# Kernel optimization log

Hardware: AMD Instinct MI355X
Metric: run time of the kernel (lower is better)

## Reference

```python
import jax, jax.numpy as jnp
import numpy as np

N_EMB = 384
BLOCK_SIZE = 256


def setup_inputs() -> dict:
    key = jax.random.key(0)
    ks = jax.random.split(key, 6)
    B, T, H, D = 256, 256, 6, 64
    x = jax.random.normal(ks[0], (B, T, N_EMB), dtype=jnp.float32)
    wk = jax.random.normal(ks[1], (H, N_EMB, D), dtype=jnp.float32) * (N_EMB ** -0.5)
    wq = jax.random.normal(ks[2], (H, N_EMB, D), dtype=jnp.float32) * (N_EMB ** -0.5)
    wv = jax.random.normal(ks[3], (H, N_EMB, D), dtype=jnp.float32) * (N_EMB ** -0.5)
    wproj = jax.random.normal(ks[4], (N_EMB, N_EMB), dtype=jnp.float32) * (N_EMB ** -0.5)
    bproj = jnp.zeros((N_EMB,), dtype=jnp.float32)
    return {"x": x, "wk": wk, "wq": wq, "wv": wv, "wproj": wproj, "bproj": bproj}


def reference(x, wk, wq, wv, wproj, bproj):
    B, T, C = x.shape  # C == N_EMB
    # per-head projections (no bias), heads stacked on leading axis
    k = jnp.einsum('btc,hcd->bhtd', x, wk)
    q = jnp.einsum('btc,hcd->bhtd', x, wq)
    v = jnp.einsum('btc,hcd->bhtd', x, wv)
    # faithful to source: wei = k @ q^T scaled by sqrt(C) (embed dim, not head dim)
    wei = jnp.einsum('bhtd,bhsd->bhts', k, q) / (C ** 0.5)
    causal = jnp.tril(jnp.ones((T, T), dtype=bool))
    wei = jnp.where(causal, wei, -jnp.inf)
    wei = jax.nn.softmax(wei, axis=-1)
    # dropout is identity in eval mode
    out = jnp.einsum('bhts,bhsd->bhtd', wei, v)  # [B,H,T,D]
    out = out.transpose(0, 2, 1, 3).reshape(B, T, C)  # concat heads
    out = out @ wproj + bproj
    return out
```

## Files before the change

### kernel.cpp

```cpp
#include <hip/hip_runtime.h>

typedef unsigned short u16;
typedef __bf16 bf16x8 __attribute__((ext_vector_type(8)));
typedef float f32x4 __attribute__((ext_vector_type(4)));

#define B_SZ 256
#define T_SZ 256
#define C_EMB 384
#define NHEAD 6
#define DHEAD 64
#define N3 1152
#define BHTD 25165824
#define SCALE 0.05103103630798287f
#define MASKV -3.0e4f

__device__ __forceinline__ u16 f2bf(float f) {
  __bf16 b = (__bf16)f;
  return __builtin_bit_cast(u16, b);
}

__device__ __forceinline__ void gload_lds16(const void* g, void* l) {
  __builtin_amdgcn_global_load_lds((const __attribute__((address_space(1))) void*)g,
                                   (__attribute__((address_space(3))) void*)l, 16, 0, 0);
}

__global__ __launch_bounds__(256) void prep_all(
    const float* __restrict__ x, const float* __restrict__ wk,
    const float* __restrict__ wq, const float* __restrict__ wv,
    const float* __restrict__ wproj,
    u16* __restrict__ xb, u16* __restrict__ wqkvt, u16* __restrict__ wprojt) {
  int bidx = blockIdx.x;
  if (bidx < 12288) {
    int i = bidx * 256 + threadIdx.x;
    float4 f0 = ((const float4*)x)[i * 2];
    float4 f1 = ((const float4*)x)[i * 2 + 1];
    uint4 p;
    p.x = (unsigned)f2bf(f0.x) | ((unsigned)f2bf(f0.y) << 16);
    p.y = (unsigned)f2bf(f0.z) | ((unsigned)f2bf(f0.w) << 16);
    p.z = (unsigned)f2bf(f1.x) | ((unsigned)f2bf(f1.y) << 16);
    p.w = (unsigned)f2bf(f1.z) | ((unsigned)f2bf(f1.w) << 16);
    ((uint4*)xb)[i] = p;
  } else {
    int i = (bidx - 12288) * 256 + threadIdx.x;
    if (i < N3 * C_EMB) {
      int n = i / C_EMB, c = i - n * C_EMB;
      int tensor = n >= 768 ? 2 : (n >= 384 ? 1 : 0);
      int r = n - tensor * 384;
      int h = r >> 6, d = r & 63;
      const float* w = tensor == 0 ? wk : (tensor == 1 ? wq : wv);
      float val = w[(h * C_EMB + c) * DHEAD + d];
      if (tensor == 0) val *= SCALE;
      wqkvt[i] = f2bf(val);
    } else {
      int ii = i - N3 * C_EMB;
      if (ii < C_EMB * C_EMB) {
        int n = ii / C_EMB, c = ii - n * C_EMB;
        wprojt[ii] = f2bf(wproj[c * C_EMB + n]);
      }
    }
  }
}

__global__ __launch_bounds__(256, 4) void qkv_gemm(const u16* __restrict__ xb,
                                                   const u16* __restrict__ wt,
                                                   u16* __restrict__ kqv) {
  __shared__ __align__(16) u16 lA[128 * 64];
  __shared__ __align__(16) u16 lB[128 * 64];
  const int tid = threadIdx.x;
  const int lane = tid & 63, w = tid >> 6;
  int bid = blockIdx.x;
  int nb = (bid & 7) * 576 + (bid >> 3);
  int mt = nb / 9, nt = nb - mt * 9;
  const int n0 = nt * 128, m0 = mt * 128;
  const int wr = w >> 1, wc = w & 1;
  f32x4 acc[4][4] = {};
  for (int kt = 0; kt < 6; ++kt) {
    const int k0 = kt * 64;
#pragma unroll
    for (int it = 0; it < 4; ++it) {
      int ub = it * 256 + w * 64;
      int u = ub + lane;
      int row = u >> 3, cu = u & 7;
      int koff = k0 + ((cu ^ (row & 7)) << 3);
      gload_lds16(xb + (size_t)(m0 + row) * C_EMB + koff, lA + ub * 8);
      gload_lds16(wt + (size_t)(n0 + row) * C_EMB + koff, lB + ub * 8);
    }
    asm volatile("s_waitcnt vmcnt(0)" ::: "memory");
    asm volatile("s_barrier" ::: "memory");
    bf16x8 af[4][2], bfr[4][2];
#pragma unroll
    for (int mi = 0; mi < 4; ++mi) {
      int row = wr * 64 + mi * 16 + (lane & 15);
#pragma unroll
      for (int kk = 0; kk < 2; ++kk) {
        int cu = kk * 4 + (lane >> 4);
        af[mi][kk] = *(const bf16x8*)((const char*)lA + row * 128 + ((cu ^ (row & 7)) << 4));
      }
    }
#pragma unroll
    for (int ni = 0; ni < 4; ++ni) {
      int row = wc * 64 + ni * 16 + (lane & 15);
#pragma unroll
      for (int kk = 0; kk < 2; ++kk) {
        int cu = kk * 4 + (lane >> 4);
        bfr[ni][kk] = *(const bf16x8*)((const char*)lB + row * 128 + ((cu ^ (row & 7)) << 4));
      }
    }
#pragma unroll
    for (int kk = 0; kk < 2; ++kk)
#pragma unroll
      for (int mi = 0; mi < 4; ++mi)
#pragma unroll
        for (int ni = 0; ni < 4; ++ni)
          acc[mi][ni] = __builtin_amdgcn_mfma_f32_16x16x32_bf16(
              af[mi][kk], bfr[ni][kk], acc[mi][ni], 0, 0, 0);
    asm volatile("s_barrier" ::: "memory");
  }

  const int tensor = nt / 3;
  if (tensor == 2) {
    u16* vt = kqv + 2 * (size_t)BHTD;
#pragma unroll
    for (int ni = 0; ni < 4; ++ni) {
      int r2 = n0 + wc * 64 + ni * 16 + (lane & 15) - 768;
      int h = r2 >> 6, d = r2 & 63;
#pragma unroll
      for (int mi = 0; mi < 4; ++mi) {
        int gm0 = m0 + wr * 64 + mi * 16 + ((lane >> 4) << 2);
        int b = gm0 >> 8, tt2 = gm0 & 255;
        ushort4 pk;
        pk.x = f2bf(acc[mi][ni][0]);
        pk.y = f2bf(acc[mi][ni][1]);
        pk.z = f2bf(acc[mi][ni][2]);
        pk.w = f2bf(acc[mi][ni][3]);
        *(ushort4*)(vt + ((size_t)(b * NHEAD + h) * 64 + d) * 256 + tt2) = pk;
      }
    }
  } else {
#pragma unroll
    for (int ni = 0; ni < 4; ++ni) {
      int gn = n0 + wc * 64 + ni * 16 + (lane & 15);
      int r2 = gn - tensor * 384;
      int h = r2 >> 6, d = r2 & 63;
#pragma unroll
      for (int mi = 0; mi < 4; ++mi) {
        int gm0 = m0 + wr * 64 + mi * 16 + ((lane >> 4) << 2);
#pragma unroll
        for (int r = 0; r < 4; ++r) {
          int m = gm0 + r;
          int b = m >> 8, t = m & 255;
          kqv[(size_t)tensor * BHTD + ((((b * NHEAD + h) << 8) + t) << 6) + d] =
              f2bf(acc[mi][ni][r]);
        }
      }
    }
  }
}

__global__ __launch_bounds__(512, 2) void attn_kernel(const u16* __restrict__ kqv,
                                                      u16* __restrict__ attnb) {
  __shared__ __align__(16) u16 lQ[256 * 64];
  __shared__ __align__(16) u16 lVt[64 * 256];
  __shared__ __align__(16) char lP[8 * 16 * 128];
  const int tid = threadIdx.x;
  const int lane = tid & 63, w = tid >> 6;
  int bid = blockIdx.x;
  const int bh = (bid & 7) * 192 + (bid >> 3);
  const u16* Kb = kqv + (size_t)bh * (T_SZ * DHEAD);
  const u16* Qb = kqv + (size_t)BHTD + (size_t)bh * (T_SZ * DHEAD);
  const u16* Vb = kqv + 2 * (size_t)BHTD + (size_t)bh * (DHEAD * T_SZ);

  const int t0w0 = w * 16;
  const int t0w1 = 240 - w * 16;
  const int tg00 = t0w0 + ((lane >> 4) << 2);
  const int tg01 = t0w1 + ((lane >> 4) << 2);

  bf16x8 af0[2], af1[2];
  {
    const u16* kr0 = Kb + (size_t)(t0w0 + (lane & 15)) * DHEAD;
    const u16* kr1 = Kb + (size_t)(t0w1 + (lane & 15)) * DHEAD;
    af0[0] = *(const bf16x8*)(kr0 + ((lane >> 4) << 3));
    af0[1] = *(const bf16x8*)(kr0 + 32 + ((lane >> 4) << 3));
    af1[0] = *(const bf16x8*)(kr1 + ((lane >> 4) << 3));
    af1[1] = *(const bf16x8*)(kr1 + 32 + ((lane >> 4) << 3));
  }
  asm volatile("" ::: "memory");
  {
    int u = tid;
    int row = u >> 3, cu = u & 7;
    gload_lds16(Qb + (size_t)row * DHEAD + ((cu ^ (row & 7)) << 3), lQ + u * 8);
  }
  asm volatile("" ::: "memory");
#pragma unroll
  for (int it = 1; it < 4; ++it) {
    int u = it * 512 + tid;
    int row = u >> 3, cu = u & 7;
    gload_lds16(Qb + (size_t)row * DHEAD + ((cu ^ (row & 7)) << 3), lQ + u * 8);
  }
  asm volatile("" ::: "memory");
#pragma unroll
  for (int it = 0; it < 4; ++it) {
    int u = it * 512 + tid;
    int row = u >> 5, cu = u & 31;
    gload_lds16(Vb + (size_t)row * T_SZ + ((cu >> 3) << 6) + (((cu & 7) ^ (row & 7)) << 3),
                lVt + u * 8);
  }
  asm volatile("s_waitcnt vmcnt(7)" ::: "memory");
  asm volatile("s_barrier" ::: "memory");

  char* lPw = lP + w * (16 * 128);
  f32x4 oacc0[4] = {}, oacc1[4] = {};
  float lrowp0[4] = {0.f, 0.f, 0.f, 0.f};
  float lrowp1[4] = {0.f, 0.f, 0.f, 0.f};
  const int last0 = t0w0 >> 6;
  const int last1 = t0w1 >> 6;

#define QK_TILE(s0_, af_, t0w_, tg0_, lrp_) { \
    f32x4 sacc[4] = {}; \
    __builtin_amdgcn_s_setprio(1); \
    _Pragma("unroll") for (int ni = 0; ni < 4; ++ni) { \
      int row = (s0_) + ni * 16 + (lane & 15); \
      _Pragma("unroll") for (int kk = 0; kk < 2; ++kk) { \
        int cu = kk * 4 + (lane >> 4); \
        bf16x8 bq = *(const bf16x8*)((const char*)lQ + row * 128 + ((cu ^ (row & 7)) << 4)); \
        sacc[ni] = __builtin_amdgcn_mfma_f32_16x16x32_bf16(af_[kk], bq, sacc[ni], 0, 0, 0); \
      } \
    } \
    __builtin_amdgcn_s_setprio(0); \
    if ((s0_) + 63 > (t0w_)) { \
      _Pragma("unroll") for (int ni = 0; ni < 4; ++ni) { \
        int sg = (s0_) + ni * 16 + (lane & 15); \
        _Pragma("unroll") for (int r = 0; r < 4; ++r) \
          if (sg > (tg0_) + r) sacc[ni][r] = MASKV; \
      } \
    } \
    _Pragma("unroll") for (int ni = 0; ni < 4; ++ni) { \
      int scol = ni * 16 + (lane & 15); \
      _Pragma("unroll") for (int r = 0; r < 4; ++r) { \
        float p = __expf(sacc[ni][r]); \
        lrp_[r] += p; \
        int trow = ((lane >> 4) << 2) + r; \
        *(u16*)(lPw + trow * 128 + ((scol * 2) ^ ((trow & 7) << 4))) = f2bf(p); \
      } \
    } }

#define PV_TILE(s0_, oacc_) { \
    bf16x8 pa[2]; \
    int trow = lane & 15; \
    _Pragma("unroll") for (int kk = 0; kk < 2; ++kk) { \
      int cu = kk * 4 + (lane >> 4); \
      pa[kk] = *(const bf16x8*)(lPw + trow * 128 + (((cu) << 4) ^ ((trow & 7) << 4))); \
    } \
    __builtin_amdgcn_s_setprio(1); \
    _Pragma("unroll") for (int nd = 0; nd < 4; ++nd) { \
      int drow = nd * 16 + (lane & 15); \
      _Pragma("unroll") for (int kk = 0; kk < 2; ++kk) { \
        int cu = kk * 4 + (lane >> 4); \
        bf16x8 vb = *(const bf16x8*)((const char*)lVt + drow * 512 + (s0_) * 2 + \
                                     (((cu) ^ (drow & 7)) << 4)); \
        oacc_[nd] = __builtin_amdgcn_mfma_f32_16x16x32_bf16(pa[kk], vb, oacc_[nd], 0, 0, 0); \
      } \
    } \
    __builtin_amdgcn_s_setprio(0); }

  QK_TILE(0, af0, t0w0, tg00, lrowp0)
  asm volatile("s_waitcnt vmcnt(0)" ::: "memory");
  asm volatile("s_barrier" ::: "memory");
  PV_TILE(0, oacc0)
  for (int si = 1; si <= last0; ++si) {
    const int s0 = si << 6;
    QK_TILE(s0, af0, t0w0, tg00, lrowp0)
    PV_TILE(s0, oacc0)
  }
  for (int si = 0; si <= last1; ++si) {
    const int s0 = si << 6;
    QK_TILE(s0, af1, t0w1, tg01, lrowp1)
    PV_TILE(s0, oacc1)
  }
#undef QK_TILE
#undef PV_TILE

#pragma unroll
  for (int r = 0; r < 4; ++r) {
#pragma unroll
    for (int off = 1; off < 16; off <<= 1) {
      lrowp0[r] += __shfl_xor(lrowp0[r], off);
      lrowp1[r] += __shfl_xor(lrowp1[r], off);
    }
  }
  const int b = bh / NHEAD, h = bh - (bh / NHEAD) * NHEAD;
#pragma unroll
  for (int r = 0; r < 4; ++r) {
    int t0_ = tg00 + r, t1_ = tg01 + r;
    float inv0 = 1.0f / lrowp0[r];
    float inv1 = 1.0f / lrowp1[r];
#pragma unroll
    for (int nd = 0; nd < 4; ++nd) {
      int col = h * 64 + nd * 16 + (lane & 15);
      attnb[((size_t)(b * T_SZ + t0_)) * C_EMB + col] = f2bf(oacc0[nd][r] * inv0);
      attnb[((size_t)(b * T_SZ + t1_)) * C_EMB + col] = f2bf(oacc1[nd][r] * inv1);
    }
  }
}

__global__ __launch_bounds__(256, 4) void out_gemm(const u16* __restrict__ a,
                                                   const u16* __restrict__ wt,
                                                   const float* __restrict__ bias,
                                                   float* __restrict__ out) {
  __shared__ __align__(16) u16 lA[128 * 64];
  __shared__ __align__(16) u16 lB[128 * 64];
  const int tid = threadIdx.x;
  const int lane = tid & 63, w = tid >> 6;
  int bid = blockIdx.x;
  int nb = (bid & 7) * 192 + (bid >> 3);
  int mt = nb / 3, nt = nb - mt * 3;
  const int n0 = nt * 128, m0 = mt * 128;
  const int wr = w >> 1, wc = w & 1;
  f32x4 acc[4][4] = {};
  for (int kt = 0; kt < 6; ++kt) {
    const int k0 = kt * 64;
#pragma unroll
    for (int it = 0; it < 4; ++it) {
      int ub = it * 256 + w * 64;
      int u = ub + lane;
      int row = u >> 3, cu = u & 7;
      int koff = k0 + ((cu ^ (row & 7)) << 3);
      gload_lds16(a + (size_t)(m0 + row) * C_EMB + koff, lA + ub * 8);
      gload_lds16(wt + (size_t)(n0 + row) * C_EMB + koff, lB + ub * 8);
    }
    asm volatile("s_waitcnt vmcnt(0)" ::: "memory");
    asm volatile("s_barrier" ::: "memory");
    bf16x8 af[4][2], bfr[4][2];
#pragma unroll
    for (int mi = 0; mi < 4; ++mi) {
      int row = wr * 64 + mi * 16 + (lane & 15);
#pragma unroll
      for (int kk = 0; kk < 2; ++kk) {
        int cu = kk * 4 + (lane >> 4);
        af[mi][kk] = *(const bf16x8*)((const char*)lA + row * 128 + ((cu ^ (row & 7)) << 4));
      }
    }
#pragma unroll
    for (int ni = 0; ni < 4; ++ni) {
      int row = wc * 64 + ni * 16 + (lane & 15);
#pragma unroll
      for (int kk = 0; kk < 2; ++kk) {
        int cu = kk * 4 + (lane >> 4);
        bfr[ni][kk] = *(const bf16x8*)((const char*)lB + row * 128 + ((cu ^ (row & 7)) << 4));
      }
    }
#pragma unroll
    for (int kk = 0; kk < 2; ++kk)
#pragma unroll
      for (int mi = 0; mi < 4; ++mi)
#pragma unroll
        for (int ni = 0; ni < 4; ++ni)
          acc[mi][ni] = __builtin_amdgcn_mfma_f32_16x16x32_bf16(
              af[mi][kk], bfr[ni][kk], acc[mi][ni], 0, 0, 0);
    asm volatile("s_barrier" ::: "memory");
  }
#pragma unroll
  for (int ni = 0; ni < 4; ++ni) {
    int gn = n0 + wc * 64 + ni * 16 + (lane & 15);
    float bv = bias[gn];
#pragma unroll
    for (int mi = 0; mi < 4; ++mi) {
      int gm0 = m0 + wr * 64 + mi * 16 + ((lane >> 4) << 2);
#pragma unroll
      for (int r = 0; r < 4; ++r)
        out[(size_t)(gm0 + r) * C_EMB + gn] = acc[mi][ni][r] + bv;
    }
  }
}

extern "C" void kernel_launch(void* const* d_in, const int* in_sizes, int n_in,
                              void* d_out, int out_size, void* d_ws, size_t ws_size,
                              hipStream_t stream) {
  const float* x = (const float*)d_in[0];
  const float* wk = (const float*)d_in[1];
  const float* wq = (const float*)d_in[2];
  const float* wv = (const float*)d_in[3];
  const float* wproj = (const float*)d_in[4];
  const float* bproj = (const float*)d_in[5];
  float* out = (float*)d_out;
  u16* ws = (u16*)d_ws;
  u16* kqv = ws;
  u16* attnb = ws + 3 * (size_t)BHTD;
  u16* xb = attnb;
  u16* wqkvt = attnb + (size_t)BHTD;
  u16* wprojt = wqkvt + (size_t)N3 * C_EMB;
  prep_all<<<14592, 256, 0, stream>>>(x, wk, wq, wv, wproj, xb, wqkvt, wprojt);
  qkv_gemm<<<4608, 256, 0, stream>>>(xb, wqkvt, kqv);
  attn_kernel<<<1536, 512, 0, stream>>>(kqv, attnb);
  out_gemm<<<1536, 256, 0, stream>>>(attnb, wprojt, bproj, out);
}
```

Before: 176.1 us.

## Software-pipeline QK and softmax/PV tiles with double-buffered score accumulators

Splits the per-tile QK matmul from the softmax+PV stage and interleaves them with two score accumulator sets, so the next tile's QK MFMAs are issued before the current tile's exp/LDS writes and PV MFMAs. The loops are fully unrolled into two fixed schedules based on the row-pair's causal extent. This is meant to hide exp/LDS latency behind MFMA work, at the cost of extra registers and hardcoded assumptions about the number of tiles per row pair.

```diff
diff --git a/kernel.cpp b/kernel.cpp
--- a/kernel.cpp
+++ b/kernel.cpp
@@ -212,73 +212,83 @@
   f32x4 oacc0[4] = {}, oacc1[4] = {};
   float lrowp0[4] = {0.f, 0.f, 0.f, 0.f};
   float lrowp1[4] = {0.f, 0.f, 0.f, 0.f};
-  const int last0 = t0w0 >> 6;
-  const int last1 = t0w1 >> 6;
-
-#define QK_TILE(s0_, af_, t0w_, tg0_, lrp_) { \
-    f32x4 sacc[4] = {}; \
+  f32x4 saccA[4], saccB[4];
+
+#define QKM(sacc_, af_, s0_) { \
+    _Pragma("unroll") for (int ni = 0; ni < 4; ++ni) \
+      sacc_[ni] = (f32x4){0.f, 0.f, 0.f, 0.f}; \
     __builtin_amdgcn_s_setprio(1); \
     _Pragma("unroll") for (int ni = 0; ni < 4; ++ni) { \
       int row = (s0_) + ni * 16 + (lane & 15); \
       _Pragma("unroll") for (int kk = 0; kk < 2; ++kk) { \
         int cu = kk * 4 + (lane >> 4); \
         bf16x8 bq = *(const bf16x8*)((const char*)lQ + row * 128 + ((cu ^ (row & 7)) << 4)); \
-        sacc[ni] = __builtin_amdgcn_mfma_f32_16x16x32_bf16(af_[kk], bq, sacc[ni], 0, 0, 0); \
+        sacc_[ni] = __builtin_amdgcn_mfma_f32_16x16x32_bf16(af_[kk], bq, sacc_[ni], 0, 0, 0); \
       } \
     } \
-    __builtin_amdgcn_s_setprio(0); \
+    __builtin_amdgcn_s_setprio(0); }
+
+#define SMPV(sacc_, s0_, t0w_, tg0_, lrp_, oacc_) { \
     if ((s0_) + 63 > (t0w_)) { \
       _Pragma("unroll") for (int ni = 0; ni < 4; ++ni) { \
         int sg = (s0_) + ni * 16 + (lane & 15); \
         _Pragma("unroll") for (int r = 0; r < 4; ++r) \
-          if (sg > (tg0_) + r) sacc[ni][r] = MASKV; \
+          if (sg > (tg0_) + r) sacc_[ni][r] = MASKV; \
       } \
     } \
     _Pragma("unroll") for (int ni = 0; ni < 4; ++ni) { \
       int scol = ni * 16 + (lane & 15); \
       _Pragma("unroll") for (int r = 0; r < 4; ++r) { \
-        float p = __expf(sacc[ni][r]); \
+        float p = __expf(sacc_[ni][r]); \
         lrp_[r] += p; \
         int trow = ((lane >> 4) << 2) + r; \
         *(u16*)(lPw + trow * 128 + ((scol * 2) ^ ((trow & 7) << 4))) = f2bf(p); \
       } \
-    } }
-
-#define PV_TILE(s0_, oacc_) { \
-    bf16x8 pa[2]; \
-    int trow = lane & 15; \
-    _Pragma("unroll") for (int kk = 0; kk < 2; ++kk) { \
-      int cu = kk * 4 + (lane >> 4); \
-      pa[kk] = *(const bf16x8*)(lPw + trow * 128 + (((cu) << 4) ^ ((trow & 7) << 4))); \
     } \
-    __builtin_amdgcn_s_setprio(1); \
-    _Pragma("unroll") for (int nd = 0; nd < 4; ++nd) { \
-      int drow = nd * 16 + (lane & 15); \
+    { bf16x8 pa[2]; \
+      int trow = lane & 15; \
       _Pragma("unroll") for (int kk = 0; kk < 2; ++kk) { \
         int cu = kk * 4 + (lane >> 4); \
-        bf16x8 vb = *(const bf16x8*)((const char*)lVt + drow * 512 + (s0_) * 2 + \
-                                     (((cu) ^ (drow & 7)) << 4)); \
-        oacc_[nd] = __builtin_amdgcn_mfma_f32_16x16x32_bf16(pa[kk], vb, oacc_[nd], 0, 0, 0); \
+        pa[kk] = *(const bf16x8*)(lPw + trow * 128 + (((cu) << 4) ^ ((trow & 7) << 4))); \
       } \
-    } \
-    __builtin_amdgcn_s_setprio(0); }
-
-  QK_TILE(0, af0, t0w0, tg00, lrowp0)
+      __builtin_amdgcn_s_setprio(1); \
+      _Pragma("unroll") for (int nd = 0; nd < 4; ++nd) { \
+        int drow = nd * 16 + (lane & 15); \
+        _Pragma("unroll") for (int kk = 0; kk < 2; ++kk) { \
+          int cu = kk * 4 + (lane >> 4); \
+          bf16x8 vb = *(const bf16x8*)((const char*)lVt + drow * 512 + (s0_) * 2 + \
+                                       (((cu) ^ (drow & 7)) << 4)); \
+          oacc_[nd] = __builtin_amdgcn_mfma_f32_16x16x32_bf16(pa[kk], vb, oacc_[nd], 0, 0, 0); \
+        } \
+      } \
+      __builtin_amdgcn_s_setprio(0); } }
+
+  QKM(saccA, af0, 0)
   asm volatile("s_waitcnt vmcnt(0)" ::: "memory");
   asm volatile("s_barrier" ::: "memory");
-  PV_TILE(0, oacc0)
-  for (int si = 1; si <= last0; ++si) {
-    const int s0 = si << 6;
-    QK_TILE(s0, af0, t0w0, tg00, lrowp0)
-    PV_TILE(s0, oacc0)
-  }
-  for (int si = 0; si <= last1; ++si) {
-    const int s0 = si << 6;
-    QK_TILE(s0, af1, t0w1, tg01, lrowp1)
-    PV_TILE(s0, oacc1)
-  }
-#undef QK_TILE
-#undef PV_TILE
+  if (t0w0 < 64) {
+    QKM(saccB, af1, 0)
+    SMPV(saccA, 0,   t0w0, tg00, lrowp0, oacc0)
+    QKM(saccA, af1, 64)
+    SMPV(saccB, 0,   t0w1, tg01, lrowp1, oacc1)
+    QKM(saccB, af1, 128)
+    SMPV(saccA, 64,  t0w1, tg01, lrowp1, oacc1)
+    QKM(saccA, af1, 192)
+    SMPV(saccB, 128, t0w1, tg01, lrowp1, oacc1)
+    SMPV(saccA, 192, t0w1, tg01, lrowp1, oacc1)
+  } else {
+    QKM(saccB, af0, 64)
+    SMPV(saccA, 0,   t0w0, tg00, lrowp0, oacc0)
+    QKM(saccA, af1, 0)
+    SMPV(saccB, 64,  t0w0, tg00, lrowp0, oacc0)
+    QKM(saccB, af1, 64)
+    SMPV(saccA, 0,   t0w1, tg01, lrowp1, oacc1)
+    QKM(saccA, af1, 128)
+    SMPV(saccB, 64,  t0w1, tg01, lrowp1, oacc1)
+    SMPV(saccA, 128, t0w1, tg01, lrowp1, oacc1)
+  }
+#undef QKM
+#undef SMPV
 
 #pragma unroll
   for (int r = 0; r < 4; ++r) {
```

Result: slower. 189.6 us (+7.7%).
